# Kernel tuning notes

Measured on AMD Instinct MI355X. Metric: run time of the kernel, lower is better.

## Reference

```python
import jax, jax.numpy as jnp
import numpy as np

DIM = 2048
H = 16
HD = 128
S = 2640          # frame_seq_len(22*40=880) * num_frame_per_block(3)
CACHE = 5280      # 6 cached frames
MAXPOS = 8192
EPS = 1e-6


def rmsnorm(x, g, eps=EPS):
    return x * jax.lax.rsqrt(jnp.mean(x * x, axis=-1, keepdims=True) + eps) * g


def apply_rope_interleaved(x, cos, sin):
    # x: [s, H, HD]; cos/sin: [s, HD//2]; is_neox=False -> adjacent pairs
    x1 = x[..., 0::2]
    x2 = x[..., 1::2]
    c = cos[:, None, :]
    s_ = sin[:, None, :]
    o1 = x1 * c - x2 * s_
    o2 = x2 * c + x1 * s_
    return jnp.stack([o1, o2], axis=-1).reshape(x.shape)


def setup_inputs() -> dict:
    key = jax.random.key(0)
    ks = jax.random.split(key, 10)
    w_scale = DIM ** -0.5
    x = jax.random.normal(ks[0], (1, S, DIM), dtype=jnp.float32)
    # cos_sin_cache: [max_pos, HD] = [cos(HD//2) | sin(HD//2)], real rope values
    inv_freq = 1.0 / (10000.0 ** (np.arange(0, HD, 2, dtype=np.float32) / HD))
    t = np.arange(MAXPOS, dtype=np.float32)
    ang = np.outer(t, inv_freq)  # [MAXPOS, HD//2]
    freqs = jnp.asarray(np.concatenate([np.cos(ang), np.sin(ang)], axis=1), dtype=jnp.float32)
    k_cache = jax.random.normal(ks[1], (CACHE, H, HD), dtype=jnp.float32)
    v_cache = jax.random.normal(ks[2], (CACHE, H, HD), dtype=jnp.float32)
    Wq = jax.random.normal(ks[3], (DIM, DIM), dtype=jnp.float32) * w_scale
    Wk = jax.random.normal(ks[4], (DIM, DIM), dtype=jnp.float32) * w_scale
    Wv = jax.random.normal(ks[5], (DIM, DIM), dtype=jnp.float32) * w_scale
    Wo = jax.random.normal(ks[6], (DIM, DIM), dtype=jnp.float32) * w_scale
    bq = jnp.zeros((DIM,), jnp.float32)
    bk = jnp.zeros((DIM,), jnp.float32)
    bv = jnp.zeros((DIM,), jnp.float32)
    bo = jnp.zeros((DIM,), jnp.float32)
    gq = jnp.ones((DIM,), jnp.float32)
    gk = jnp.ones((DIM,), jnp.float32)
    return {"x": x, "freqs": freqs, "k_cache": k_cache, "v_cache": v_cache,
            "Wq": Wq, "bq": bq, "Wk": Wk, "bk": bk, "Wv": Wv, "bv": bv,
            "Wo": Wo, "bo": bo, "gq": gq, "gk": gk, "current_start": CACHE}


def reference(x, freqs, k_cache, v_cache, Wq, bq, Wk, bk, Wv, bv, Wo, bo, gq, gk, current_start):
    s = x.shape[1]
    xf = x[0]                                   # [s, DIM], B==1
    q = rmsnorm(xf @ Wq.T + bq, gq).reshape(s, H, HD)
    k = rmsnorm(xf @ Wk.T + bk, gk).reshape(s, H, HD)
    v = (xf @ Wv.T + bv).reshape(s, H, HD)
    # fused RoPE via cos_sin_cache lookup, interleaved (is_neox=False)
    positions = jnp.arange(s, dtype=jnp.int32) + current_start
    cs = freqs[positions]                       # [s, HD]
    cos, sin = cs[:, : HD // 2], cs[:, HD // 2:]
    rq = apply_rope_interleaved(q, cos, sin)
    rk = apply_rope_interleaved(k, cos, sin)
    # streaming attention: full access to cache, causal within incoming block
    k_all = jnp.concatenate([k_cache, rk], axis=0)  # [L, H, HD]
    v_all = jnp.concatenate([v_cache, v], axis=0)
    L = k_all.shape[0]
    scale = HD ** -0.5
    scores = jnp.einsum("qhd,khd->hqk", rq, k_all) * scale  # [H, s, L]
    kv_idx = jnp.arange(L)
    q_idx = jnp.arange(s)
    mask = (kv_idx[None, :] - (L - s)) <= q_idx[:, None]    # cache always visible
    scores = jnp.where(mask[None, :, :], scores, jnp.float32(-1e30))
    attn = jax.nn.softmax(scores, axis=-1)
    out = jnp.einsum("hqk,khd->qhd", attn, v_all).reshape(s, DIM)
    y = out @ Wo.T + bo
    return y[None]                              # [1, s, DIM]
```

## Files before the change

kernel.cpp:

```cpp
#include <hip/hip_runtime.h>

#define DIMN 2048
#define NH 16
#define HDIM 128

typedef __attribute__((ext_vector_type(4))) float f32x4;
typedef __attribute__((ext_vector_type(8))) __bf16 bfx8;
typedef __attribute__((ext_vector_type(8))) unsigned short u16x8;
typedef __attribute__((ext_vector_type(4))) unsigned short u16x4;

__device__ __forceinline__ unsigned short f2bf(float f){
  unsigned u = __builtin_bit_cast(unsigned, f);
  u += 0x7fffu + ((u >> 16) & 1u);
  return (unsigned short)(u >> 16);
}

__device__ __forceinline__ void gl_lds16(const void* g, void* l){
  __builtin_amdgcn_global_load_lds((const __attribute__((address_space(1))) void*)g,
                                   (__attribute__((address_space(3))) void*)l, 16, 0, 0);
}

#define MFMA16(a,b,c) __builtin_amdgcn_mfma_f32_16x16x32_bf16((a),(b),(c),0,0,0)

__global__ __launch_bounds__(256) void cast_bf16_kernel(const float* __restrict__ in,
                                                        unsigned short* __restrict__ out, int n8){
  int i = blockIdx.x*256 + threadIdx.x;
  if (i >= n8) return;
  const float4* p = (const float4*)(in + (size_t)i*8);
  float4 a = p[0], b = p[1];
  u16x8 o;
  o[0]=f2bf(a.x); o[1]=f2bf(a.y); o[2]=f2bf(a.z); o[3]=f2bf(a.w);
  o[4]=f2bf(b.x); o[5]=f2bf(b.y); o[6]=f2bf(b.z); o[7]=f2bf(b.w);
  *(u16x8*)(out + (size_t)i*8) = o;
}

__global__ __launch_bounds__(256) void kcache_kernel(const float* __restrict__ kc,
                                                     unsigned short* __restrict__ kb,
                                                     int R, int L_){
  const int gid = blockIdx.x*256 + threadIdx.x;
  if (gid >= R*256) return;
  const size_t idx = (size_t)gid * 8;
  const int k   = (int)(idx >> 11);
  const int rem = (int)(idx & 2047);
  const int hh  = rem >> 7, d = rem & 127;
  const float4* p = (const float4*)(kc + idx);
  float4 a = p[0], b = p[1];
  u16x8 o;
  o[0]=f2bf(a.x); o[1]=f2bf(a.y); o[2]=f2bf(a.z); o[3]=f2bf(a.w);
  o[4]=f2bf(b.x); o[5]=f2bf(b.y); o[6]=f2bf(b.z); o[7]=f2bf(b.w);
  *(u16x8*)(kb + (size_t)hh*L_*HDIM + (size_t)k*HDIM + d) = o;
}

__global__ __launch_bounds__(256) void vtrans_kernel(const float* __restrict__ src,
                                                     unsigned short* __restrict__ vt,
                                                     int R, int koff, int L_){
  __shared__ __align__(16) unsigned short tile[32][72];
  const int kb0 = blockIdx.x * 64, db0 = blockIdx.y * 32, hh = blockIdx.z;
  const int t = threadIdx.x;
  const int kk = t >> 2, dd = (t & 3) * 8;
  const int k = kb0 + kk;
  if (k < R){
    const float* p = src + (size_t)k*DIMN + hh*HDIM + db0 + dd;
    float4 a = ((const float4*)p)[0], b = ((const float4*)p)[1];
    tile[dd+0][kk] = f2bf(a.x); tile[dd+1][kk] = f2bf(a.y);
    tile[dd+2][kk] = f2bf(a.z); tile[dd+3][kk] = f2bf(a.w);
    tile[dd+4][kk] = f2bf(b.x); tile[dd+5][kk] = f2bf(b.y);
    tile[dd+6][kk] = f2bf(b.z); tile[dd+7][kk] = f2bf(b.w);
  }
  __syncthreads();
  const int d = t >> 3, k0 = (t & 7) * 8;
  unsigned short* dst = vt + (size_t)hh*HDIM*L_ + (size_t)(db0+d)*L_ + koff + kb0 + k0;
  if (kb0 + k0 + 8 <= R){
    *(u16x8*)dst = *(const u16x8*)&tile[d][k0];
  } else {
    #pragma unroll
    for (int e=0;e<8;++e) if (kb0 + k0 + e < R) dst[e] = tile[d][k0+e];
  }
}

__global__ __launch_bounds__(256) void norm_rope_kernel(const float* __restrict__ lin,
    const float* __restrict__ g, const float* __restrict__ freqs, const int* __restrict__ cur,
    unsigned short* __restrict__ out, int S_, size_t head_stride, int row_off){
  const int q = blockIdx.x, t = threadIdx.x;
  const float* row = lin + (size_t)q * DIMN;
  float4 v0 = ((const float4*)row)[t*2];
  float4 v1 = ((const float4*)row)[t*2+1];
  float x[8] = {v0.x, v0.y, v0.z, v0.w, v1.x, v1.y, v1.z, v1.w};
  float ss = 0.f;
  #pragma unroll
  for (int e=0;e<8;++e) ss += x[e]*x[e];
  for (int m=1;m<64;m<<=1) ss += __shfl_xor(ss, m);
  __shared__ float red[4];
  if ((t & 63) == 0) red[t>>6] = ss;
  __syncthreads();
  const float tot = red[0]+red[1]+red[2]+red[3];
  const float rstd = rsqrtf(tot * (1.0f/2048.0f) + 1e-6f);
  const int n0 = t*8;
  float xr[8];
  #pragma unroll
  for (int e=0;e<8;++e) xr[e] = x[e] * rstd * g[n0+e];
  const int pos = cur[0] + q;
  const int hh = n0 >> 7, d0 = n0 & 127;
  const float* fr = freqs + (size_t)pos * HDIM;
  float o[8];
  #pragma unroll
  for (int p=0;p<4;++p){
    const int j = (d0>>1) + p;
    const float c = fr[j], s = fr[64+j];
    o[2*p]   = xr[2*p]*c - xr[2*p+1]*s;
    o[2*p+1] = xr[2*p+1]*c + xr[2*p]*s;
  }
  u16x8 ov;
  #pragma unroll
  for (int e=0;e<8;++e) ov[e] = f2bf(o[e]);
  *(u16x8*)(out + (size_t)hh*head_stride + (size_t)(q+row_off)*HDIM + d0) = ov;
}

__global__ __launch_bounds__(256,2) void gemm_bt(const unsigned short* __restrict__ A,
    const unsigned short* __restrict__ B, const float* __restrict__ bias,
    float* __restrict__ C, int M, int N, int K){
  __shared__ __align__(16) unsigned short As[128*64];
  __shared__ __align__(16) unsigned short Bs[128*64];
  const int t = threadIdx.x;
  const int w = t >> 6, lane = t & 63, lh = lane >> 4, ll = lane & 15;
  const int wr = w >> 1, wc = w & 1;
  const int m0 = blockIdx.y * 128, n0 = blockIdx.x * 128;
  const int srow = t >> 3;
  const int scb  = (t & 7) * 16;
  const int swc  = (scb ^ ((srow & 7) << 4)) >> 1;
  int arow[4]; size_t brow[4];
  #pragma unroll
  for (int c=0;c<4;++c){
    int r = m0 + c*32 + srow; if (r >= M) r = M-1;
    arow[c] = r;
    brow[c] = (size_t)(n0 + c*32 + srow);
  }
  const int xsw = (ll & 7) << 4;
  f32x4 acc[4][4] = {};
  const int nk = K >> 6;
  for (int kt = 0; kt < nk; ++kt){
    const int k0 = kt << 6;
    #pragma unroll
    for (int c=0;c<4;++c){
      gl_lds16(A + (size_t)arow[c]*K + k0 + swc, (char*)As + c*4096 + w*1024);
      gl_lds16(B + brow[c]*K       + k0 + swc, (char*)Bs + c*4096 + w*1024);
    }
    asm volatile("s_waitcnt vmcnt(0)" ::: "memory");
    __syncthreads();
    #pragma unroll
    for (int kk=0;kk<2;++kk){
      const int cb = kk*64 + lh*16;
      bfx8 a[4], b[4];
      #pragma unroll
      for (int i=0;i<4;++i)
        a[i] = *(const bfx8*)((const char*)As + (wr*64 + i*16 + ll)*128 + (cb ^ xsw));
      #pragma unroll
      for (int j=0;j<4;++j)
        b[j] = *(const bfx8*)((const char*)Bs + (wc*64 + j*16 + ll)*128 + (cb ^ xsw));
      #pragma unroll
      for (int i=0;i<4;++i)
        #pragma unroll
        for (int j=0;j<4;++j)
          acc[i][j] = MFMA16(a[i], b[j], acc[i][j]);
    }
    __syncthreads();
  }
  #pragma unroll
  for (int i=0;i<4;++i){
    #pragma unroll
    for (int j=0;j<4;++j){
      const int col = n0 + wc*64 + j*16 + ll;
      const float bb = bias[col];
      #pragma unroll
      for (int r=0;r<4;++r){
        const int row = m0 + wr*64 + i*16 + lh*4 + r;
        if (row < M) C[(size_t)row*N + col] = acc[i][j][r] + bb;
      }
    }
  }
}

__global__ __launch_bounds__(256,2) void attn_kernel(const unsigned short* __restrict__ Q,
    const unsigned short* __restrict__ K, const unsigned short* __restrict__ VT,
    unsigned short* __restrict__ O, float* __restrict__ pacc, float* __restrict__ pml,
    int S_, int L_, int CLn, int nsplit){
  __shared__ __align__(16) unsigned short Ks[64*128];
  __shared__ __align__(16) unsigned short Vs[128*64];
  const int hh = blockIdx.y;
  const int q0 = blockIdx.x * 128;
  const int z  = blockIdx.z;
  const int t = threadIdx.x, w = t >> 6, lane = t & 63, lh = lane >> 4, ll = lane & 15;
  const int xsw = (ll & 7) << 4;
  char* Pw = (char*)Ks + w*4096;
  const unsigned short* Qh = Q  + (size_t)hh*S_*HDIM;
  const unsigned short* Kh = K  + (size_t)hh*L_*HDIM;
  const unsigned short* Vh = VT + (size_t)hh*HDIM*L_;
  bfx8 qf[2][4];
  #pragma unroll
  for (int i=0;i<2;++i){
    int qr = q0 + w*32 + i*16 + ll; if (qr >= S_) qr = S_ - 1;
    #pragma unroll
    for (int kk=0;kk<4;++kk)
      qf[i][kk] = *(const bfx8*)(Qh + (size_t)qr*HDIM + kk*32 + lh*8);
  }
  f32x4 acc[2][8] = {};
  float m_st[2], l_st[2];
  m_st[0] = m_st[1] = -1e20f;
  l_st[0] = l_st[1] = 0.f;
  const int wrow0 = q0 + w*32;
  int qlast = q0 + 127; if (qlast >= S_) qlast = S_ - 1;
  const int kend = CLn + qlast + 1;
  const int nt = (kend + 63) >> 6;
  const int tps = (nt + nsplit - 1) / nsplit;
  const int t0 = z * tps;
  int t1 = t0 + tps; if (t1 > nt) t1 = nt;
  const float scale = 0.08838834764831845f;
  const int ksrow = t >> 4, kchunk = t & 15;
  const int vsrow = t >> 3, vchunk = t & 7;
  const int myq[2] = { wrow0 + ll, wrow0 + 16 + ll };

  u16x8 kreg[4], vreg[4];
  auto load_tile = [&](int ktile){
    const int kv0 = ktile << 6;
    #pragma unroll
    for (int c=0;c<4;++c){
      int krow = kv0 + c*16 + ksrow; if (krow >= L_) krow = L_ - 1;
      kreg[c] = *(const u16x8*)(Kh + (size_t)krow*HDIM + kchunk*8);
      int vcol = kv0 + vchunk*8; if (vcol > L_ - 8) vcol = L_ - 8;
      vreg[c] = *(const u16x8*)(Vh + (size_t)(c*32 + vsrow)*L_ + vcol);
    }
  };
  if (t0 < t1) load_tile(t0);

  for (int kt = t0; kt < t1; ++kt){
    const int kv0 = kt << 6;
    __syncthreads();
    #pragma unroll
    for (int c=0;c<4;++c){
      *(u16x8*)((char*)Ks + (c*16 + ksrow)*256 + ((kchunk*16) ^ ((ksrow & 7) << 4))) = kreg[c];
      *(u16x8*)((char*)Vs + (c*32 + vsrow)*128 + ((vchunk*16) ^ ((vsrow & 7) << 4))) = vreg[c];
    }
    __syncthreads();
    if (kt + 1 < t1) load_tile(kt + 1);
    f32x4 sc[2][4] = {};
    #pragma unroll
    for (int kk=0;kk<4;++kk){
      const int cb = kk*64 + lh*16;
      #pragma unroll
      for (int j=0;j<4;++j){
        bfx8 kf = *(const bfx8*)((const char*)Ks + (j*16 + ll)*256 + (cb ^ xsw));
        sc[0][j] = MFMA16(kf, qf[0][kk], sc[0][j]);
        sc[1][j] = MFMA16(kf, qf[1][kk], sc[1][j]);
      }
    }
    const bool needmask = (kv0 + 63 > CLn + wrow0);
    if (needmask){
      #pragma unroll
      for (int i=0;i<2;++i){
        const int lim = CLn + myq[i];
        #pragma unroll
        for (int j=0;j<4;++j)
          #pragma unroll
          for (int r=0;r<4;++r){
            const int key = kv0 + j*16 + lh*4 + r;
            sc[i][j][r] = (key > lim) ? -1e30f : sc[i][j][r]*scale;
          }
      }
    } else {
      #pragma unroll
      for (int i=0;i<2;++i)
        #pragma unroll
        for (int j=0;j<4;++j)
          #pragma unroll
          for (int r=0;r<4;++r) sc[i][j][r] *= scale;
    }
    float m_t[2];
    #pragma unroll
    for (int i=0;i<2;++i){
      float mt = sc[i][0][0];
      #pragma unroll
      for (int j=0;j<4;++j)
        #pragma unroll
        for (int r=0;r<4;++r) mt = fmaxf(mt, sc[i][j][r]);
      mt = fmaxf(mt, __shfl_xor(mt, 16));
      mt = fmaxf(mt, __shfl_xor(mt, 32));
      m_t[i] = fmaxf(mt, -1e20f);
    }
    const float mdiff = fmaxf(m_t[0] - m_st[0], m_t[1] - m_st[1]);
    if (!__all(mdiff <= 8.0f)){
      float corr[2];
      #pragma unroll
      for (int i=0;i<2;++i){
        const float mn = fmaxf(m_st[i], m_t[i]);
        corr[i] = __expf(m_st[i] - mn);
        m_st[i] = mn;
        l_st[i] *= corr[i];
      }
      #pragma unroll
      for (int i=0;i<2;++i)
        #pragma unroll
        for (int r=0;r<4;++r){
          const float ca = __shfl(corr[i], lh*4 + r);
          #pragma unroll
          for (int jn=0;jn<8;++jn) acc[i][jn][r] *= ca;
        }
    }
    #pragma unroll
    for (int i=0;i<2;++i){
      float rs = 0.f;
      #pragma unroll
      for (int j=0;j<4;++j)
        #pragma unroll
        for (int r=0;r<4;++r){
          const float pv = __expf(sc[i][j][r] - m_st[i]);
          sc[i][j][r] = pv;
          rs += pv;
        }
      rs += __shfl_xor(rs, 16);
      rs += __shfl_xor(rs, 32);
      l_st[i] += rs;
    }
    __syncthreads();
    #pragma unroll
    for (int i=0;i<2;++i)
      #pragma unroll
      for (int j=0;j<4;++j){
        u16x4 pk;
        #pragma unroll
        for (int r=0;r<4;++r) pk[r] = f2bf(sc[i][j][r]);
        *(u16x4*)(Pw + (i*16 + ll)*128 + ((j*32 + lh*8) ^ xsw)) = pk;
      }
    #pragma unroll
    for (int kk=0;kk<2;++kk){
      const int cb = kk*64 + lh*16;
      bfx8 af0 = *(const bfx8*)(Pw + (ll)*128      + (cb ^ xsw));
      bfx8 af1 = *(const bfx8*)(Pw + (16 + ll)*128 + (cb ^ xsw));
      #pragma unroll
      for (int jn=0;jn<8;++jn){
        bfx8 vf = *(const bfx8*)((const char*)Vs + (jn*16 + ll)*128 + (cb ^ xsw));
        acc[0][jn] = MFMA16(af0, vf, acc[0][jn]);
        acc[1][jn] = MFMA16(af1, vf, acc[1][jn]);
      }
    }
  }
  if (nsplit == 1){
    #pragma unroll
    for (int i=0;i<2;++i){
      const float linv = 1.0f / l_st[i];
      #pragma unroll
      for (int r=0;r<4;++r){
        const float inv = __shfl(linv, lh*4 + r);
        const int qr = wrow0 + i*16 + lh*4 + r;
        if (qr < S_){
          #pragma unroll
          for (int jn=0;jn<8;++jn)
            O[(size_t)qr*DIMN + hh*HDIM + jn*16 + ll] = f2bf(acc[i][jn][r]*inv);
        }
      }
    }
  } else {
    #pragma unroll
    for (int i=0;i<2;++i){
      #pragma unroll
      for (int r=0;r<4;++r){
        const int qr = wrow0 + i*16 + lh*4 + r;
        if (qr < S_){
          const size_t rid = ((size_t)z*NH + hh)*S_ + qr;
          float* dst = pacc + rid*128;
          #pragma unroll
          for (int jn=0;jn<8;++jn) dst[jn*16 + ll] = acc[i][jn][r];
        }
      }
      if (lane < 16){
        const int qr2 = myq[i];
        if (qr2 < S_){
          const size_t rid2 = ((size_t)z*NH + hh)*S_ + qr2;
          pml[rid2*2]   = m_st[i];
          pml[rid2*2+1] = l_st[i];
        }
      }
    }
  }
}

__global__ __launch_bounds__(256) void combine_kernel(const float* __restrict__ pacc,
    const float* __restrict__ pml, unsigned short* __restrict__ ob, int S_, int nsplit){
  const int t = threadIdx.x;
  const int rid = blockIdx.x*2 + (t >> 7);
  if (rid >= S_*NH) return;
  const int d = t & 127;
  const int hh = rid / S_;
  const int q  = rid - hh*S_;
  float M = -1e20f;
  for (int s=0; s<nsplit; ++s)
    M = fmaxf(M, pml[((size_t)s*NH*S_ + rid)*2]);
  float lt = 0.f, o = 0.f;
  for (int s=0; s<nsplit; ++s){
    const float m = pml[((size_t)s*NH*S_ + rid)*2];
    const float l = pml[((size_t)s*NH*S_ + rid)*2 + 1];
    const float wgt = __expf(m - M);
    lt += l * wgt;
    o  += pacc[((size_t)s*NH*S_ + rid)*128 + d] * wgt;
  }
  if (lt == 0.f) lt = 1.f;
  ob[(size_t)q*DIMN + hh*HDIM + d] = f2bf(o / lt);
}

extern "C" void kernel_launch(void* const* d_in, const int* in_sizes, int n_in,
                              void* d_out, int out_size, void* d_ws, size_t ws_size,
                              hipStream_t stream){
  const float* x       = (const float*)d_in[0];
  const float* freqs   = (const float*)d_in[1];
  const float* k_cache = (const float*)d_in[2];
  const float* v_cache = (const float*)d_in[3];
  const float* Wq = (const float*)d_in[4];
  const float* bq = (const float*)d_in[5];
  const float* Wk = (const float*)d_in[6];
  const float* bk = (const float*)d_in[7];
  const float* Wv = (const float*)d_in[8];
  const float* bv = (const float*)d_in[9];
  const float* Wo = (const float*)d_in[10];
  const float* bo = (const float*)d_in[11];
  const float* gq = (const float*)d_in[12];
  const float* gk = (const float*)d_in[13];
  const int*   cur = (const int*)d_in[14];

  const int S = in_sizes[0] / DIMN;
  const int CACHE_ = in_sizes[2] / DIMN;
  const int L = CACHE_ + S;
  const int CLn = L - S;

  auto al = [](size_t n){ return (n + 255) & ~(size_t)255; };
  char* base = (char*)d_ws;
  size_t off = 0;
  auto take = [&](size_t n){ char* r = base + off; off += al(n); return r; };
  unsigned short* xb  = (unsigned short*)take((size_t)S*DIMN*2);
  unsigned short* Wob = (unsigned short*)take((size_t)DIMN*DIMN*2);
  unsigned short* qb  = (unsigned short*)take((size_t)NH*S*HDIM*2);
  unsigned short* kb  = (unsigned short*)take((size_t)NH*L*HDIM*2);
  unsigned short* vtb = (unsigned short*)take((size_t)NH*HDIM*L*2);
  unsigned short* ob  = (unsigned short*)take((size_t)S*DIMN*2);
  const size_t ubase = off;
  const size_t lin_sz = al((size_t)S*DIMN*4);
  const size_t w_sz   = al((size_t)DIMN*DIMN*2);
  float*          lin = (float*)(base + ubase);
  unsigned short* Wqb = (unsigned short*)(base + ubase + lin_sz);
  unsigned short* Wkb = (unsigned short*)(base + ubase + lin_sz + w_sz);
  unsigned short* Wvb = (unsigned short*)(base + ubase + lin_sz + 2*w_sz);
  const size_t trans_sz = lin_sz + 3*w_sz;
  auto pool_sz = [&](int ns){
    return al((size_t)ns*NH*S*HDIM*4) + al((size_t)ns*NH*S*2*4);
  };
  int nsplit = 1;
  if (ubase + (trans_sz > pool_sz(4) ? trans_sz : pool_sz(4)) <= ws_size) nsplit = 4;
  else if (ubase + (trans_sz > pool_sz(2) ? trans_sz : pool_sz(2)) <= ws_size) nsplit = 2;
  if (ubase + trans_sz > ws_size) return;
  float* pacc = (float*)(base + ubase);
  float* pml  = (float*)(base + ubase + al((size_t)nsplit*NH*S*HDIM*4));

  const int wn8 = DIMN*DIMN/8;
  cast_bf16_kernel<<<(S*DIMN/8+255)/256, 256, 0, stream>>>(x,  xb,  S*DIMN/8);
  cast_bf16_kernel<<<(wn8+255)/256, 256, 0, stream>>>(Wq, Wqb, wn8);
  cast_bf16_kernel<<<(wn8+255)/256, 256, 0, stream>>>(Wk, Wkb, wn8);
  cast_bf16_kernel<<<(wn8+255)/256, 256, 0, stream>>>(Wv, Wvb, wn8);
  cast_bf16_kernel<<<(wn8+255)/256, 256, 0, stream>>>(Wo, Wob, wn8);
  kcache_kernel<<<CACHE_, 256, 0, stream>>>(k_cache, kb, CACHE_, L);
  vtrans_kernel<<<dim3((CACHE_+63)/64, 4, NH), 256, 0, stream>>>(v_cache, vtb, CACHE_, 0, L);

  dim3 ggrid(DIMN/128, (S+127)/128);
  gemm_bt<<<ggrid, 256, 0, stream>>>(xb, Wqb, bq, lin, S, DIMN, DIMN);
  norm_rope_kernel<<<S, 256, 0, stream>>>(lin, gq, freqs, cur, qb, S, (size_t)S*HDIM, 0);
  gemm_bt<<<ggrid, 256, 0, stream>>>(xb, Wkb, bk, lin, S, DIMN, DIMN);
  norm_rope_kernel<<<S, 256, 0, stream>>>(lin, gk, freqs, cur, kb, S, (size_t)L*HDIM, CACHE_);
  gemm_bt<<<ggrid, 256, 0, stream>>>(xb, Wvb, bv, lin, S, DIMN, DIMN);
  vtrans_kernel<<<dim3((S+63)/64, 4, NH), 256, 0, stream>>>(lin, vtb, S, CACHE_, L);

  attn_kernel<<<dim3((S+127)/128, NH, nsplit), 256, 0, stream>>>(qb, kb, vtb, ob,
                                                                 pacc, pml, S, L, CLn, nsplit);
  if (nsplit > 1)
    combine_kernel<<<(S*NH+1)/2, 256, 0, stream>>>(pacc, pml, ob, S, nsplit);
  gemm_bt<<<ggrid, 256, 0, stream>>>(ob, Wob, bo, (float*)d_out, S, DIMN, DIMN);
}
```

Before: 534.6 us.

## Batch QKV projections into one bf16-output GEMM and double-buffer attention K/V tiles

The three separate Q/K/V GEMMs become one batched launch (grid z=3), and each writes bf16 intermediates instead of fp32. Norm-rope and the V transpose now read bf16, which halves intermediate traffic and fills the GPU better with 3x more blocks. The attention kernel gains double-buffered K/V LDS tiles and a separate P buffer, which removes one barrier per tile and overlaps staging with compute. The cost is much more LDS per block, which may reduce occupancy, and the pre-norm values are now rounded to bf16.

```diff
diff --git a/kernel.cpp b/kernel.cpp
--- a/kernel.cpp
+++ b/kernel.cpp
@@ -13,6 +13,10 @@
   unsigned u = __builtin_bit_cast(unsigned, f);
   u += 0x7fffu + ((u >> 16) & 1u);
   return (unsigned short)(u >> 16);
+}
+__device__ __forceinline__ float bf2f(unsigned short h){
+  unsigned u = (unsigned)h << 16;
+  return __builtin_bit_cast(float, u);
 }
 
 __device__ __forceinline__ void gl_lds16(const void* g, void* l){
@@ -78,14 +82,37 @@
   }
 }
 
-__global__ __launch_bounds__(256) void norm_rope_kernel(const float* __restrict__ lin,
+__global__ __launch_bounds__(256) void vtrans_bf16_kernel(const unsigned short* __restrict__ src,
+    unsigned short* __restrict__ vt, int R, int koff, int L_){
+  __shared__ __align__(16) unsigned short tile[32][72];
+  const int kb0 = blockIdx.x * 64, db0 = blockIdx.y * 32, hh = blockIdx.z;
+  const int t = threadIdx.x;
+  const int kk = t >> 2, dd = (t & 3) * 8;
+  const int k = kb0 + kk;
+  if (k < R){
+    u16x8 a = *(const u16x8*)(src + (size_t)k*DIMN + hh*HDIM + db0 + dd);
+    #pragma unroll
+    for (int e=0;e<8;++e) tile[dd+e][kk] = a[e];
+  }
+  __syncthreads();
+  const int d = t >> 3, k0 = (t & 7) * 8;
+  unsigned short* dst = vt + (size_t)hh*HDIM*L_ + (size_t)(db0+d)*L_ + koff + kb0 + k0;
+  if (kb0 + k0 + 8 <= R){
+    *(u16x8*)dst = *(const u16x8*)&tile[d][k0];
+  } else {
+    #pragma unroll
+    for (int e=0;e<8;++e) if (kb0 + k0 + e < R) dst[e] = tile[d][k0+e];
+  }
+}
+
+__global__ __launch_bounds__(256) void norm_rope_kernel(const unsigned short* __restrict__ lin,
     const float* __restrict__ g, const float* __restrict__ freqs, const int* __restrict__ cur,
     unsigned short* __restrict__ out, int S_, size_t head_stride, int row_off){
   const int q = blockIdx.x, t = threadIdx.x;
-  const float* row = lin + (size_t)q * DIMN;
-  float4 v0 = ((const float4*)row)[t*2];
-  float4 v1 = ((const float4*)row)[t*2+1];
-  float x[8] = {v0.x, v0.y, v0.z, v0.w, v1.x, v1.y, v1.z, v1.w};
+  u16x8 v = *(const u16x8*)(lin + (size_t)q*DIMN + t*8);
+  float x[8];
+  #pragma unroll
+  for (int e=0;e<8;++e) x[e] = bf2f(v[e]);
   float ss = 0.f;
   #pragma unroll
   for (int e=0;e<8;++e) ss += x[e]*x[e];
@@ -180,18 +207,90 @@
   }
 }
 
+__global__ __launch_bounds__(256,2) void gemm_qkv(const unsigned short* __restrict__ A,
+    const unsigned short* __restrict__ B0, const unsigned short* __restrict__ B1,
+    const unsigned short* __restrict__ B2, const float* __restrict__ g0,
+    const float* __restrict__ g1, const float* __restrict__ g2,
+    unsigned short* __restrict__ C0, unsigned short* __restrict__ C1,
+    unsigned short* __restrict__ C2, int M, int N, int K){
+  const int zz = blockIdx.z;
+  const unsigned short* B = (zz==0) ? B0 : (zz==1) ? B1 : B2;
+  const float* bias       = (zz==0) ? g0 : (zz==1) ? g1 : g2;
+  unsigned short* C       = (zz==0) ? C0 : (zz==1) ? C1 : C2;
+  __shared__ __align__(16) unsigned short As[128*64];
+  __shared__ __align__(16) unsigned short Bs[128*64];
+  const int t = threadIdx.x;
+  const int w = t >> 6, lane = t & 63, lh = lane >> 4, ll = lane & 15;
+  const int wr = w >> 1, wc = w & 1;
+  const int m0 = blockIdx.y * 128, n0 = blockIdx.x * 128;
+  const int srow = t >> 3;
+  const int scb  = (t & 7) * 16;
+  const int swc  = (scb ^ ((srow & 7) << 4)) >> 1;
+  int arow[4]; size_t brow[4];
+  #pragma unroll
+  for (int c=0;c<4;++c){
+    int r = m0 + c*32 + srow; if (r >= M) r = M-1;
+    arow[c] = r;
+    brow[c] = (size_t)(n0 + c*32 + srow);
+  }
+  const int xsw = (ll & 7) << 4;
+  f32x4 acc[4][4] = {};
+  const int nk = K >> 6;
+  for (int kt = 0; kt < nk; ++kt){
+    const int k0 = kt << 6;
+    #pragma unroll
+    for (int c=0;c<4;++c){
+      gl_lds16(A + (size_t)arow[c]*K + k0 + swc, (char*)As + c*4096 + w*1024);
+      gl_lds16(B + brow[c]*K       + k0 + swc, (char*)Bs + c*4096 + w*1024);
+    }
+    asm volatile("s_waitcnt vmcnt(0)" ::: "memory");
+    __syncthreads();
+    #pragma unroll
+    for (int kk=0;kk<2;++kk){
+      const int cb = kk*64 + lh*16;
+      bfx8 a[4], b[4];
+      #pragma unroll
+      for (int i=0;i<4;++i)
+        a[i] = *(const bfx8*)((const char*)As + (wr*64 + i*16 + ll)*128 + (cb ^ xsw));
+      #pragma unroll
+      for (int j=0;j<4;++j)
+        b[j] = *(const bfx8*)((const char*)Bs + (wc*64 + j*16 + ll)*128 + (cb ^ xsw));
+      #pragma unroll
+      for (int i=0;i<4;++i)
+        #pragma unroll
+        for (int j=0;j<4;++j)
+          acc[i][j] = MFMA16(a[i], b[j], acc[i][j]);
+    }
+    __syncthreads();
+  }
+  #pragma unroll
+  for (int i=0;i<4;++i){
+    #pragma unroll
+    for (int j=0;j<4;++j){
+      const int col = n0 + wc*64 + j*16 + ll;
+      const float bb = bias[col];
+      #pragma unroll
+      for (int r=0;r<4;++r){
+        const int row = m0 + wr*64 + i*16 + lh*4 + r;
+        if (row < M) C[(size_t)row*N + col] = f2bf(acc[i][j][r] + bb);
+      }
+    }
+  }
+}
+
 __global__ __launch_bounds__(256,2) void attn_kernel(const unsigned short* __restrict__ Q,
     const unsigned short* __restrict__ K, const unsigned short* __restrict__ VT,
     unsigned short* __restrict__ O, float* __restrict__ pacc, float* __restrict__ pml,
     int S_, int L_, int CLn, int nsplit){
-  __shared__ __align__(16) unsigned short Ks[64*128];
-  __shared__ __align__(16) unsigned short Vs[128*64];
+  __shared__ __align__(16) unsigned short Ks[2][64*128];
+  __shared__ __align__(16) unsigned short Vs[2][128*64];
+  __shared__ __align__(16) unsigned short Ps[4][32*64];
   const int hh = blockIdx.y;
   const int q0 = blockIdx.x * 128;
   const int z  = blockIdx.z;
   const int t = threadIdx.x, w = t >> 6, lane = t & 63, lh = lane >> 4, ll = lane & 15;
   const int xsw = (ll & 7) << 4;
-  char* Pw = (char*)Ks + w*4096;
+  char* Pw = (char*)Ps[w];
   const unsigned short* Qh = Q  + (size_t)hh*S_*HDIM;
   const unsigned short* Kh = K  + (size_t)hh*L_*HDIM;
   const unsigned short* Vh = VT + (size_t)hh*HDIM*L_;
@@ -230,28 +329,38 @@
       vreg[c] = *(const u16x8*)(Vh + (size_t)(c*32 + vsrow)*L_ + vcol);
     }
   };
-  if (t0 < t1) load_tile(t0);
-
+  auto stage_write = [&](int b){
+    #pragma unroll
+    for (int c=0;c<4;++c){
+      *(u16x8*)((char*)Ks[b] + (c*16 + ksrow)*256 + ((kchunk*16) ^ ((ksrow & 7) << 4))) = kreg[c];
+      *(u16x8*)((char*)Vs[b] + (c*32 + vsrow)*128 + ((vchunk*16) ^ ((vsrow & 7) << 4))) = vreg[c];
+    }
+  };
+  if (t0 < t1){
+    load_tile(t0);
+    stage_write(0);
+    if (t0 + 1 < t1) load_tile(t0 + 1);
+  }
+  int cur = 0;
   for (int kt = t0; kt < t1; ++kt){
     const int kv0 = kt << 6;
     __syncthreads();
-    #pragma unroll
-    for (int c=0;c<4;++c){
-      *(u16x8*)((char*)Ks + (c*16 + ksrow)*256 + ((kchunk*16) ^ ((ksrow & 7) << 4))) = kreg[c];
-      *(u16x8*)((char*)Vs + (c*32 + vsrow)*128 + ((vchunk*16) ^ ((vsrow & 7) << 4))) = vreg[c];
-    }
-    __syncthreads();
-    if (kt + 1 < t1) load_tile(kt + 1);
+    const char* Kc = (const char*)Ks[cur];
+    const char* Vc = (const char*)Vs[cur];
     f32x4 sc[2][4] = {};
     #pragma unroll
     for (int kk=0;kk<4;++kk){
       const int cb = kk*64 + lh*16;
       #pragma unroll
       for (int j=0;j<4;++j){
-        bfx8 kf = *(const bfx8*)((const char*)Ks + (j*16 + ll)*256 + (cb ^ xsw));
+        bfx8 kf = *(const bfx8*)(Kc + (j*16 + ll)*256 + (cb ^ xsw));
         sc[0][j] = MFMA16(kf, qf[0][kk], sc[0][j]);
         sc[1][j] = MFMA16(kf, qf[1][kk], sc[1][j]);
       }
+    }
+    if (kt + 1 < t1){
+      stage_write(cur ^ 1);
+      if (kt + 2 < t1) load_tile(kt + 2);
     }
     const bool needmask = (kv0 + 63 > CLn + wrow0);
     if (needmask){
@@ -320,7 +429,6 @@
       rs += __shfl_xor(rs, 32);
       l_st[i] += rs;
     }
-    __syncthreads();
     #pragma unroll
     for (int i=0;i<2;++i)
       #pragma unroll
@@ -337,11 +445,12 @@
       bfx8 af1 = *(const bfx8*)(Pw + (16 + ll)*128 + (cb ^ xsw));
       #pragma unroll
       for (int jn=0;jn<8;++jn){
-        bfx8 vf = *(const bfx8*)((const char*)Vs + (jn*16 + ll)*128 + (cb ^ xsw));
+        bfx8 vf = *(const bfx8*)(Vc + (jn*16 + ll)*128 + (cb ^ xsw));
         acc[0][jn] = MFMA16(af0, vf, acc[0][jn]);
         acc[1][jn] = MFMA16(af1, vf, acc[1][jn]);
       }
     }
+    cur ^= 1;
   }
   if (nsplit == 1){
     #pragma unroll
@@ -441,13 +550,15 @@
   unsigned short* vtb = (unsigned short*)take((size_t)NH*HDIM*L*2);
   unsigned short* ob  = (unsigned short*)take((size_t)S*DIMN*2);
   const size_t ubase = off;
-  const size_t lin_sz = al((size_t)S*DIMN*4);
-  const size_t w_sz   = al((size_t)DIMN*DIMN*2);
-  float*          lin = (float*)(base + ubase);
-  unsigned short* Wqb = (unsigned short*)(base + ubase + lin_sz);
-  unsigned short* Wkb = (unsigned short*)(base + ubase + lin_sz + w_sz);
-  unsigned short* Wvb = (unsigned short*)(base + ubase + lin_sz + 2*w_sz);
-  const size_t trans_sz = lin_sz + 3*w_sz;
+  const size_t l_sz = al((size_t)S*DIMN*2);
+  const size_t w_sz = al((size_t)DIMN*DIMN*2);
+  unsigned short* lin0 = (unsigned short*)(base + ubase);
+  unsigned short* lin1 = (unsigned short*)(base + ubase + l_sz);
+  unsigned short* lin2 = (unsigned short*)(base + ubase + 2*l_sz);
+  unsigned short* Wqb  = (unsigned short*)(base + ubase + 3*l_sz);
+  unsigned short* Wkb  = (unsigned short*)(base + ubase + 3*l_sz + w_sz);
+  unsigned short* Wvb  = (unsigned short*)(base + ubase + 3*l_sz + 2*w_sz);
+  const size_t trans_sz = 3*l_sz + 3*w_sz;
   auto pool_sz = [&](int ns){
     return al((size_t)ns*NH*S*HDIM*4) + al((size_t)ns*NH*S*2*4);
   };
@@ -467,17 +578,16 @@
   kcache_kernel<<<CACHE_, 256, 0, stream>>>(k_cache, kb, CACHE_, L);
   vtrans_kernel<<<dim3((CACHE_+63)/64, 4, NH), 256, 0, stream>>>(v_cache, vtb, CACHE_, 0, L);
 
-  dim3 ggrid(DIMN/128, (S+127)/128);
-  gemm_bt<<<ggrid, 256, 0, stream>>>(xb, Wqb, bq, lin, S, DIMN, DIMN);
-  norm_rope_kernel<<<S, 256, 0, stream>>>(lin, gq, freqs, cur, qb, S, (size_t)S*HDIM, 0);
-  gemm_bt<<<ggrid, 256, 0, stream>>>(xb, Wkb, bk, lin, S, DIMN, DIMN);
-  norm_rope_kernel<<<S, 256, 0, stream>>>(lin, gk, freqs, cur, kb, S, (size_t)L*HDIM, CACHE_);
-  gemm_bt<<<ggrid, 256, 0, stream>>>(xb, Wvb, bv, lin, S, DIMN, DIMN);
-  vtrans_kernel<<<dim3((S+63)/64, 4, NH), 256, 0, stream>>>(lin, vtb, S, CACHE_, L);
+  const int mb = (S+127)/128;
+  gemm_qkv<<<dim3(DIMN/128, mb, 3), 256, 0, stream>>>(xb, Wqb, Wkb, Wvb, bq, bk, bv,
+                                                      lin0, lin1, lin2, S, DIMN, DIMN);
+  norm_rope_kernel<<<S, 256, 0, stream>>>(lin0, gq, freqs, cur, qb, S, (size_t)S*HDIM, 0);
+  norm_rope_kernel<<<S, 256, 0, stream>>>(lin1, gk, freqs, cur, kb, S, (size_t)L*HDIM, CACHE_);
+  vtrans_bf16_kernel<<<dim3((S+63)/64, 4, NH), 256, 0, stream>>>(lin2, vtb, S, CACHE_, L);
 
   attn_kernel<<<dim3((S+127)/128, NH, nsplit), 256, 0, stream>>>(qb, kb, vtb, ob,
                                                                  pacc, pml, S, L, CLn, nsplit);
   if (nsplit > 1)
     combine_kernel<<<(S*NH+1)/2, 256, 0, stream>>>(pacc, pml, ob, S, nsplit);
-  gemm_bt<<<ggrid, 256, 0, stream>>>(ob, Wob, bo, (float*)d_out, S, DIMN, DIMN);
-}
+  gemm_bt<<<dim3(DIMN/128, mb), 256, 0, stream>>>(ob, Wob, bo, (float*)d_out, S, DIMN, DIMN);
+}
```

Measured after the change: 504.5 us. -5.6%, faster.
